# Performance work log

Hardware: AMD Instinct MI355X
Metric: run time of the kernel (lower is better)

## Reference

```python
import jax, jax.numpy as jnp
import numpy as np
import math

N_NODES = 20000
N_EDGES = 320000
NODE_IN = 128
HIDDEN = 64
HEADS = 4
TIME_DIM = 64
SCALE = 60.0 / 1.0  # sensitivity / epsilon


def _linear_params(key, din, dout):
    k1, k2 = jax.random.split(key)
    bound = 1.0 / math.sqrt(din)
    w = jax.random.uniform(k1, (din, dout), minval=-bound, maxval=bound, dtype=jnp.float32)
    b = jax.random.uniform(k2, (dout,), minval=-bound, maxval=bound, dtype=jnp.float32)
    return w, b


def setup_inputs() -> dict:
    key = jax.random.key(0)
    ks = jax.random.split(key, 16)
    edge_index = jax.random.randint(ks[0], (2, N_EDGES), 0, N_NODES, dtype=jnp.int64)
    raw_time = jax.random.uniform(ks[1], (N_EDGES, 1), dtype=jnp.float32) * 86400.0
    noise = jax.random.laplace(ks[2], (N_EDGES, 1), dtype=jnp.float32) * SCALE
    node_emb = jax.random.normal(ks[3], (N_NODES, NODE_IN), dtype=jnp.float32)
    HC = HEADS * HIDDEN
    wq1, bq1 = _linear_params(ks[4], NODE_IN, HC)
    wk1, bk1 = _linear_params(ks[5], NODE_IN, HC)
    wv1, bv1 = _linear_params(ks[6], NODE_IN, HC)
    wt1, bt1 = _linear_params(ks[7], TIME_DIM, HC)
    wq2, bq2 = _linear_params(ks[8], HC, HC)
    wk2, bk2 = _linear_params(ks[9], HC, HC)
    wv2, bv2 = _linear_params(ks[10], HC, HC)
    wt2, bt2 = _linear_params(ks[11], TIME_DIM, HC)
    wc, bc = _linear_params(ks[12], HC, 1)
    return dict(edge_index=edge_index, raw_time=raw_time, noise=noise, node_emb=node_emb,
                wq1=wq1, bq1=bq1, wk1=wk1, bk1=bk1, wv1=wv1, bv1=bv1, wt1=wt1, bt1=bt1,
                wq2=wq2, bq2=bq2, wk2=wk2, bk2=bk2, wv2=wv2, bv2=bv2, wt2=wt2, bt2=bt2,
                wc=wc, bc=bc)


def time_encode(t):
    # t: [E, 1] -> [E, TIME_DIM]; interleaved sin/cos as in TimeEncoder
    half = jnp.arange(0, TIME_DIM, 2, dtype=jnp.float32)
    div_term = jnp.exp(half * (-math.log(10000.0) / TIME_DIM))  # [TIME_DIM/2]
    arg = t * div_term  # [E, TIME_DIM/2]
    te = jnp.stack([jnp.sin(arg), jnp.cos(arg)], axis=-1)  # [E, T/2, 2]
    return te.reshape(t.shape[0], TIME_DIM)


def temporal_conv(x, src, dst, time_enc, wq, bq, wk, bk, wv, bv, wt, bt):
    # gather-QKV, edge softmax over dst segments, scatter-add aggregation
    N = x.shape[0]
    q = (x @ wq + bq).reshape(N, HEADS, HIDDEN)
    k = (x @ wk + bk).reshape(N, HEADS, HIDDEN)
    v = (x @ wv + bv).reshape(N, HEADS, HIDDEN)
    t_enc = (time_enc @ wt + bt).reshape(-1, HEADS, HIDDEN)  # [E,H,C]
    q_i = q[dst]                      # [E,H,C]
    k_j = k[src] + t_enc              # [E,H,C]
    alpha = (q_i * k_j).sum(-1) / math.sqrt(HIDDEN)  # [E,H]
    # segment softmax over index = dst (PyG softmax semantics)
    amax = jax.ops.segment_max(alpha, dst, num_segments=N)  # [N,H]
    ea = jnp.exp(alpha - amax[dst])
    denom = jax.ops.segment_sum(ea, dst, num_segments=N)
    alpha = ea / (denom[dst] + 1e-16)
    msg = v[src] * alpha[..., None]   # [E,H,C]
    out = jax.ops.segment_sum(msg, dst, num_segments=N)  # [N,H,C]
    return out.reshape(N, HEADS * HIDDEN)


def reference(edge_index, raw_time, noise, node_emb,
              wq1, bq1, wk1, bk1, wv1, bv1, wt1, bt1,
              wq2, bq2, wk2, bk2, wv2, bv2, wt2, bt2,
              wc, bc):
    src, dst = edge_index[0], edge_index[1]
    noisy_time = raw_time + noise                 # Laplace mechanism
    time_encoded = time_encode(noisy_time)        # [E, TIME_DIM]
    x = jax.nn.relu(temporal_conv(node_emb, src, dst, time_encoded,
                                  wq1, bq1, wk1, bk1, wv1, bv1, wt1, bt1))
    x = jax.nn.relu(temporal_conv(x, src, dst, time_encoded,
                                  wq2, bq2, wk2, bk2, wv2, bv2, wt2, bt2))
    edge_emb = x[src] + x[dst]                    # [E, H*C]
    out = edge_emb @ wc + bc                      # [E, 1]
    return out.squeeze(-1)
```

## Files before the change

### kernel.cpp

```cpp
#include <hip/hip_runtime.h>
#include <hip/hip_fp16.h>
#include <math.h>

#define NN   20000
#define NE   320000
#define NIN  128
#define HC   256
#define NB   1024

#define AGG_BLOCKS 2500
#define AGG_STRIDE 10000
#define LOG2E_8    0.18033688f

#define GEMM_BLOCKS 1280
#define GEMM_RT     157

typedef unsigned short u16;
typedef __attribute__((ext_vector_type(8))) short bf16x8;
typedef __attribute__((ext_vector_type(4))) float f32x4;

__device__ __forceinline__ float bf2f(u16 u) {
  union { unsigned int i; float f; } x;
  x.i = ((unsigned int)u) << 16;
  return x.f;
}
__device__ __forceinline__ u16 f2bf(float f) {
  union { float f; unsigned int i; } x;
  x.f = f;
  unsigned int r = x.i + 0x7fffu + ((x.i >> 16) & 1u);
  return (u16)(r >> 16);
}
__device__ __forceinline__ float bflo(int v) {
  union { int i; float f; } x; x.i = v << 16; return x.f;
}
__device__ __forceinline__ float bfhi(int v) {
  union { int i; float f; } x; x.i = v & 0xffff0000; return x.f;
}

__device__ __forceinline__ float ldf(const void* p, int i, bool fbf) {
  return fbf ? bf2f(((const u16*)p)[i]) : ((const float*)p)[i];
}
__device__ __forceinline__ int ldsrc(const void* p, int e, bool is64) {
  const int* p32 = (const int*)p;
  return is64 ? p32[2 * e] : p32[e];
}
__device__ __forceinline__ int lddst(const void* p, int e, bool is64) {
  const int* p32 = (const int*)p;
  return is64 ? p32[2 * (NE + e)] : p32[NE + e];
}
__device__ __forceinline__ void stout(void* p, int i, float v, bool fbf) {
  if (fbf) ((u16*)p)[i] = f2bf(v);
  else ((float*)p)[i] = v;
}

__device__ __forceinline__ void gload_lds16(const u16* g, u16* l) {
  __builtin_amdgcn_global_load_lds(
      (const __attribute__((address_space(1))) void*)g,
      (__attribute__((address_space(3))) void*)l, 16, 0, 0);
}

__device__ __forceinline__ float dpp_row_allsum(float s) {
  union fi { float f; int i; };
  fi a, b;
  a.f = s;
  b.i = __builtin_amdgcn_update_dpp(0, a.i, 0x121, 0xf, 0xf, true); a.f += b.f;
  b.i = __builtin_amdgcn_update_dpp(0, a.i, 0x122, 0xf, 0xf, true); a.f += b.f;
  b.i = __builtin_amdgcn_update_dpp(0, a.i, 0x124, 0xf, 0xf, true); a.f += b.f;
  b.i = __builtin_amdgcn_update_dpp(0, a.i, 0x128, 0xf, 0xf, true); a.f += b.f;
  return a.f;
}

__device__ __forceinline__ float fexp2(float x) {
#if __has_builtin(__builtin_amdgcn_exp2f)
  return __builtin_amdgcn_exp2f(x);
#else
  return exp2f(x);
#endif
}

#if __has_builtin(__builtin_amdgcn_fdot2_f32_bf16)
#define HAS_BF16_DOT2 1
typedef __attribute__((ext_vector_type(2))) __bf16 bfv2_t;
__device__ __forceinline__ float qkdot2(int a, int b, float c) {
  return __builtin_amdgcn_fdot2_f32_bf16(__builtin_bit_cast(bfv2_t, a),
                                         __builtin_bit_cast(bfv2_t, b), c, false);
}
#else
#define HAS_BF16_DOT2 0
#endif

__device__ __forceinline__ void edge_do(int2 kk, int2 vv, float tt, int2 q2,
    float dc0, float dc1,
    float qsx, float qsy, float qsz, float qsw,
    float px, float py, float pz, float pw, float qb,
    float& denom, float& a0, float& a1, float& a2, float& a3) {
  const float CH = 0.15915494f;
  const float CL = (float)(0.15915494309189535 - (double)0.15915494f);
  float x0 = tt * dc0, x1 = tt * dc1;
  float p0 = x0 * CH, p1 = x1 * CH;
  float e0 = fmaf(x0, CH, -p0), e1 = fmaf(x1, CH, -p1);
  e0 = fmaf(x0, CL, e0);  e1 = fmaf(x1, CL, e1);
  float fr0 = (p0 - rintf(p0)) + e0;
  float fr1 = (p1 - rintf(p1)) + e1;
  float sv0 = __builtin_amdgcn_sinf(fr0), cv0 = __builtin_amdgcn_cosf(fr0);
  float sv1 = __builtin_amdgcn_sinf(fr1), cv1 = __builtin_amdgcn_cosf(fr1);
  float stp = sv0 * px + cv0 * py + sv1 * pz + cv1 * pw;
#if HAS_BF16_DOT2
  float sqk = qkdot2(kk.y, q2.y, qkdot2(kk.x, q2.x, 0.f));
  float partial = sqk * LOG2E_8 + stp;
#else
  float partial = stp + qsx * bflo(kk.x) + qsy * bfhi(kk.x) +
                  qsz * bflo(kk.y) + qsw * bfhi(kk.y);
#endif
  float a = dpp_row_allsum(partial) + qb;
  float ea = fexp2(a);
  denom += ea;
  a0 = fmaf(ea, bflo(vv.x), a0);
  a1 = fmaf(ea, bfhi(vv.x), a1);
  a2 = fmaf(ea, bflo(vv.y), a2);
  a3 = fmaf(ea, bfhi(vv.y), a3);
}

__global__ void devinit_zero_kernel(const void* __restrict__ eidx,
                                    const void* __restrict__ nemb,
                                    int* __restrict__ flags, float* __restrict__ divt,
                                    int* __restrict__ cursor) {
  int i = blockIdx.x * 256 + threadIdx.x;
  if (i < NN) cursor[i] = 0;
  if (blockIdx.x == 0) {
    int lane = threadIdx.x;
    if (lane < 32) {
      const float c32 = (float)(-0.14391156831212787);
      float prod = (float)(2 * lane) * c32;
      divt[lane] = (float)exp((double)prod);
    }
    if (lane == 0) {
      const int* p32 = (const int*)eidx;
      int is64 = 1;
      for (int k = 1; k < 128; k += 2)
        if (p32[k] != 0) { is64 = 0; break; }
      const u16* q16 = (const u16*)nemb;
      int fbf = 1;
      for (int k = 0; k < 128; k += 2) {
        unsigned e = (q16[k] >> 7) & 0xFF;
        if (e < 90 || e > 140) { fbf = 0; break; }
      }
      flags[0] = is64;
      flags[1] = fbf;
    }
  }
}

__global__ void sentinel_kernel(const int* __restrict__ flags, void* __restrict__ out) {
  int i = blockIdx.x * 256 + threadIdx.x;
  if (i < NE) stout(out, i, 3000.0f, flags[1] != 0);
}
__global__ void raw_sentinel_kernel(u16* __restrict__ out) {
  int i = blockIdx.x * 256 + threadIdx.x;
  if (i < NE) out[i] = f2bf(3000.0f);
}

__global__ void hist_cast_kernel(const int* __restrict__ flags, const void* __restrict__ eidx,
                                 int* __restrict__ cnt, const void* __restrict__ nemb,
                                 u16* __restrict__ acast) {
  bool is64 = flags[0] != 0;
  int b = blockIdx.x, t = threadIdx.x;
  if (b < (NE / 256)) {
    int e = b * 256 + t;
    int d = lddst(eidx, e, is64);
    if ((unsigned)d < NN) atomicAdd(&cnt[d], 1);
  }
  if (!flags[1]) {
    int i = b * 256 + t;
    if (i < NN * NIN / 4) {
      float4 v = ((const float4*)nemb)[i];
      ushort4 o;
      o.x = f2bf(v.x); o.y = f2bf(v.y); o.z = f2bf(v.z); o.w = f2bf(v.w);
      ((ushort4*)acast)[i] = o;
    }
  }
}

__global__ __launch_bounds__(1024) void scanall_kernel(int* __restrict__ cnt_cursor,
                                                       int* __restrict__ offs) {
  __shared__ int s[1024];
  int t = threadIdx.x;
  const int PER = (NN + 1023) / 1024;
  int base = t * PER;
  int loc[PER];
  int sum = 0;
#pragma unroll
  for (int i = 0; i < PER; ++i) {
    int idx = base + i;
    int v = (idx < NN) ? cnt_cursor[idx] : 0;
    loc[i] = sum;
    sum += v;
  }
  s[t] = sum;
  __syncthreads();
  for (int off = 1; off < 1024; off <<= 1) {
    int y = (t >= off) ? s[t - off] : 0;
    __syncthreads();
    s[t] += y;
    __syncthreads();
  }
  int tbase = s[t] - sum;
#pragma unroll
  for (int i = 0; i < PER; ++i) {
    int idx = base + i;
    if (idx < NN) {
      int v = tbase + loc[i];
      offs[idx] = v;
      cnt_cursor[idx] = v;
    }
  }
  if (t == 1023) offs[NN] = s[t];
}

__global__ void fill_kernel(const int* __restrict__ flags, const void* __restrict__ eidx,
                            const void* __restrict__ rawt, const void* __restrict__ noise,
                            int* __restrict__ cursor, int* __restrict__ ssrc,
                            float* __restrict__ stt) {
  bool is64 = flags[0] != 0, fbf = flags[1] != 0;
  int e = blockIdx.x * 256 + threadIdx.x;
  if (e < NE) {
    int d = lddst(eidx, e, is64);
    if ((unsigned)d < NN) {
      int pos = atomicAdd(&cursor[d], 1);
      if ((unsigned)pos < NE) {
        int src = ldsrc(eidx, e, is64);
        if ((unsigned)src >= NN) src = 0;
        ssrc[pos] = src;
        stt[pos] = ldf(rawt, e, fbf) + ldf(noise, e, fbf);
      }
    }
  }
}

__global__ void transw3_kernel(const int* __restrict__ flags, const void* __restrict__ W0,
                               const void* __restrict__ W1, const void* __restrict__ W2,
                               u16* __restrict__ WtBig, int K) {
  bool fbf = flags[1] != 0;
  __shared__ u16 tile[64][65];
  int z = blockIdx.z;
  const void* W = (z == 0) ? W0 : (z == 1) ? W1 : W2;
  u16* dst = WtBig + (size_t)z * 256 * K;
  int kb = blockIdx.x * 64, cb = blockIdx.y * 64;
  int tx = threadIdx.x & 63, ty = threadIdx.x >> 6;
  for (int i = ty; i < 64; i += 4)
    tile[tx][i] = f2bf(ldf(W, (kb + i) * HC + cb + tx, fbf));
  __syncthreads();
  for (int i = ty; i < 64; i += 4)
    dst[(size_t)(cb + i) * K + kb + tx] = tile[i][tx];
}

__global__ void wcombbias_kernel(const int* __restrict__ flags, const void* __restrict__ wt,
                                 const u16* __restrict__ Wqt, u16* __restrict__ Wout,
                                 const void* __restrict__ bq, const void* __restrict__ bk,
                                 const void* __restrict__ bv, float* __restrict__ biasBig,
                                 int K) {
  bool fbf = flags[1] != 0;
  int b = blockIdx.x, t = threadIdx.x;
  if (b < 256) {
    __shared__ float wrow[64];
    int j = b, h = j >> 6;
    if (t < 64) wrow[t] = ldf(wt, (j & 63) * HC + h * 64 + t, fbf);
    __syncthreads();
    if (t < K) {
      float s = 0.f;
#pragma unroll 8
      for (int mm = 0; mm < 64; ++mm)
        s += wrow[mm] * bf2f(Wqt[(size_t)(h * 64 + mm) * K + t]);
      Wout[(size_t)j * K + t] = f2bf(s);
    }
  } else if (b < 259) {
    int bb = b - 256;
    const void* p = (bb == 0) ? bq : (bb == 1) ? bk : bv;
    biasBig[bb * 256 + t] = ldf(p, t, fbf);
  } else {
    int j = t, h = j >> 6;
    float s = 0.f;
    for (int mm = 0; mm < 64; ++mm)
      s += ldf(bq, h * 64 + mm, fbf) * ldf(wt, (j & 63) * HC + h * 64 + mm, fbf);
    biasBig[768 + j] = s;
  }
}

template <int KT, bool AWS>
__global__ __launch_bounds__(256) void gemm_mfma(
    const int* __restrict__ flags, const void* __restrict__ Ap,
    const u16* __restrict__ Acast, const u16* __restrict__ Wt,
    const float* __restrict__ bias, u16* __restrict__ C, int M) {
  bool fbf = flags[1] != 0;
  const u16* A = AWS ? (const u16*)Ap : (fbf ? (const u16*)Ap : Acast);

  int lid = blockIdx.x;
  int xcd = lid & 7;
  int j = lid >> 3;
  int rl = j >> 3, col = j & 7;
  const int qr = GEMM_RT >> 3, rem = GEMM_RT & 7;
  int nrows = qr + (xcd < rem ? 1 : 0);
  if (rl >= nrows) return;
  int row = xcd * qr + (xcd < rem ? xcd : rem) + rl;
  int rb = row * 128, cb = col * 128;

  __shared__ u16 As[128 * 128];
  __shared__ u16 Bs[128 * 128];
  int tid = threadIdx.x;
  int wave = tid >> 6, lane = tid & 63;
  int l15 = lane & 15, quad = lane >> 4;
  int mbase = (wave >> 1) * 64, nbase = (wave & 1) * 64;

  f32x4 acc[4][4];
#pragma unroll
  for (int mt = 0; mt < 4; ++mt)
#pragma unroll
    for (int nt = 0; nt < 4; ++nt)
#pragma unroll
      for (int r = 0; r < 4; ++r) acc[mt][nt][r] = 0.f;

  int srow0 = tid >> 2, schunk0 = tid & 3;
  int srow1 = (tid + 256) >> 2, schunk1 = (tid + 256) & 3;
  int gchunk0 = schunk0 ^ (srow0 & 3);
  int gchunk1 = schunk1 ^ (srow1 & 3);
  int arow0 = rb + srow0; if (arow0 >= M) arow0 = M - 1;
  int arow1 = rb + srow1; if (arow1 >= M) arow1 = M - 1;
  int slo0 = srow0 * 32 + schunk0 * 8;
  int slo1 = srow1 * 32 + schunk1 * 8;
  const u16* bsrc0 = Wt + (size_t)(cb + srow0) * KT + gchunk0 * 8;
  const u16* bsrc1 = Wt + (size_t)(cb + srow1) * KT + gchunk1 * 8;
  const u16* asrc0 = A + (size_t)arow0 * KT + gchunk0 * 8;
  const u16* asrc1 = A + (size_t)arow1 * KT + gchunk1 * 8;

#pragma unroll
  for (int sl = 0; sl < KT / 128; ++sl) {
    if (sl) __syncthreads();
#pragma unroll
    for (int s = 0; s < 4; ++s) {
      int kk = sl * 128 + s * 32;
      int sb = s * 4096;
      gload_lds16(asrc0 + kk, &As[sb + slo0]);
      gload_lds16(asrc1 + kk, &As[sb + slo1]);
      gload_lds16(bsrc0 + kk, &Bs[sb + slo0]);
      gload_lds16(bsrc1 + kk, &Bs[sb + slo1]);
    }
    __syncthreads();
#pragma unroll
    for (int s = 0; s < 4; ++s) {
      int sb = s * 4096;
      bf16x8 bfrag[4];
#pragma unroll
      for (int nt = 0; nt < 4; ++nt) {
        int col2 = nbase + nt * 16 + l15;
        bfrag[nt] = *(const bf16x8*)&Bs[sb + col2 * 32 + ((quad ^ (col2 & 3)) * 8)];
      }
#pragma unroll
      for (int mt = 0; mt < 4; ++mt) {
        int row2 = mbase + mt * 16 + l15;
        bf16x8 afrag = *(const bf16x8*)&As[sb + row2 * 32 + ((quad ^ (row2 & 3)) * 8)];
#pragma unroll
        for (int nt = 0; nt < 4; ++nt)
          acc[mt][nt] = __builtin_amdgcn_mfma_f32_16x16x32_bf16(afrag, bfrag[nt], acc[mt][nt], 0, 0, 0);
      }
    }
  }

  float bvv[4];
#pragma unroll
  for (int nt = 0; nt < 4; ++nt) bvv[nt] = bias[cb + nbase + nt * 16 + l15];
#pragma unroll
  for (int mt = 0; mt < 4; ++mt) {
#pragma unroll
    for (int r = 0; r < 4; ++r) {
      int grow = rb + mbase + mt * 16 + quad * 4 + r;
      if (grow < M) {
        size_t rowo = (size_t)grow * NB + cb + nbase + l15;
#pragma unroll
        for (int nt = 0; nt < 4; ++nt)
          C[rowo + nt * 16] = f2bf(acc[mt][nt][r] + bvv[nt]);
      }
    }
  }
}

template <int DOY>
__global__ __launch_bounds__(256) void aggfused_kernel(
    const int* __restrict__ flags, const int* __restrict__ ssrc,
    const int* __restrict__ offsets, const float* __restrict__ stt,
    const float* __restrict__ divt,
    const u16* __restrict__ qkvp, const void* __restrict__ bt,
    u16* __restrict__ xout, const void* __restrict__ wc,
    float* __restrict__ ynode) {
  bool fbf = flags[1] != 0;
  int lane = threadIdx.x & 63;
  int c = lane * 4;

  int i0 = (2 * lane) & 31;
  float dc0 = divt[i0], dc1 = divt[i0 + 1];
  float btv0 = ldf(bt, c + 0, fbf), btv1 = ldf(bt, c + 1, fbf);
  float btv2 = ldf(bt, c + 2, fbf), btv3 = ldf(bt, c + 3, fbf);
  float wcv0 = 0.f, wcv1 = 0.f, wcv2 = 0.f, wcv3 = 0.f;
  if (DOY) {
    wcv0 = ldf(wc, c + 0, fbf); wcv1 = ldf(wc, c + 1, fbf);
    wcv2 = ldf(wc, c + 2, fbf); wcv3 = ldf(wc, c + 3, fbf);
  }

  int n = blockIdx.x * 4 + (threadIdx.x >> 6);
  int s0 = offsets[n], s1 = offsets[n + 1];
  int2 q2 = *(const int2*)(qkvp + (size_t)n * NB + c);
  int2 p2 = *(const int2*)(qkvp + (size_t)n * NB + 768 + c);

  while (n < NN) {
    int n1 = n + AGG_STRIDE;
    int n1c = (n1 < NN) ? n1 : 0;
    int s0n = offsets[n1c], s1n = offsets[n1c + 1];
    int2 q2n = *(const int2*)(qkvp + (size_t)n1c * NB + c);
    int2 p2n = *(const int2*)(qkvp + (size_t)n1c * NB + 768 + c);

    float qx = bflo(q2.x), qy = bfhi(q2.x), qz = bflo(q2.y), qw = bfhi(q2.y);
    float px = bflo(p2.x) * LOG2E_8, py = bfhi(p2.x) * LOG2E_8;
    float pz = bflo(p2.y) * LOG2E_8, pw = bfhi(p2.y) * LOG2E_8;
    float pb = qx * btv0 + qy * btv1 + qz * btv2 + qw * btv3;
    float qb = dpp_row_allsum(pb) * LOG2E_8;
    float qsx = qx * LOG2E_8, qsy = qy * LOG2E_8;
    float qsz = qz * LOG2E_8, qsw = qw * LOG2E_8;

    float denom = 0.f, acc0 = 0.f, acc1 = 0.f, acc2 = 0.f, acc3 = 0.f;
    const int* sp = ssrc + s0;
    const float* tp = stt + s0;
    int ecnt = s1 - s0;
    int e = 0;
    if (ecnt >= 4) {
      int sA = sp[0], sB = sp[1], sC = sp[2], sD = sp[3];
      while (e + 4 <= ecnt) {
        const u16* bA = qkvp + ((unsigned)sA << 10) + c;
        const u16* bB = qkvp + ((unsigned)sB << 10) + c;
        const u16* bC = qkvp + ((unsigned)sC << 10) + c;
        const u16* bD = qkvp + ((unsigned)sD << 10) + c;
        int2 kA = *(const int2*)(bA + 256), vA = *(const int2*)(bA + 512);
        int2 kB = *(const int2*)(bB + 256), vB = *(const int2*)(bB + 512);
        int2 kC = *(const int2*)(bC + 256), vC = *(const int2*)(bC + 512);
        int2 kD = *(const int2*)(bD + 256), vD = *(const int2*)(bD + 512);
        float ttA = tp[e], ttB = tp[e + 1], ttC = tp[e + 2], ttD = tp[e + 3];
        int en = e + 4;
        if (en + 4 <= ecnt) {
          sA = sp[en]; sB = sp[en + 1]; sC = sp[en + 2]; sD = sp[en + 3];
        }
        edge_do(kA, vA, ttA, q2, dc0, dc1, qsx, qsy, qsz, qsw, px, py, pz, pw, qb,
                denom, acc0, acc1, acc2, acc3);
        edge_do(kB, vB, ttB, q2, dc0, dc1, qsx, qsy, qsz, qsw, px, py, pz, pw, qb,
                denom, acc0, acc1, acc2, acc3);
        edge_do(kC, vC, ttC, q2, dc0, dc1, qsx, qsy, qsz, qsw, px, py, pz, pw, qb,
                denom, acc0, acc1, acc2, acc3);
        edge_do(kD, vD, ttD, q2, dc0, dc1, qsx, qsy, qsz, qsw, px, py, pz, pw, qb,
                denom, acc0, acc1, acc2, acc3);
        e = en;
      }
    }
    for (; e < ecnt; ++e) {
      int s = sp[e];
      const u16* bS = qkvp + ((unsigned)s << 10) + c;
      int2 kS = *(const int2*)(bS + 256), vS = *(const int2*)(bS + 512);
      float tt = tp[e];
      edge_do(kS, vS, tt, q2, dc0, dc1, qsx, qsy, qsz, qsw, px, py, pz, pw, qb,
              denom, acc0, acc1, acc2, acc3);
    }

    float inv = 1.f / (denom + 1e-16f);
    ushort4 r;
    r.x = f2bf(fmaxf(acc0 * inv, 0.f));
    r.y = f2bf(fmaxf(acc1 * inv, 0.f));
    r.z = f2bf(fmaxf(acc2 * inv, 0.f));
    r.w = f2bf(fmaxf(acc3 * inv, 0.f));
    *(ushort4*)(xout + (size_t)n * HC + c) = r;
    if (DOY) {
      float yv = bf2f(r.x) * wcv0 + bf2f(r.y) * wcv1 +
                 bf2f(r.z) * wcv2 + bf2f(r.w) * wcv3;
      yv = dpp_row_allsum(yv);
      yv += __shfl_xor(yv, 16);
      yv += __shfl_xor(yv, 32);
      if (lane == 0) ynode[n] = yv;
    }

    n = n1;
    s0 = s0n; s1 = s1n; q2 = q2n; p2 = p2n;
  }
}

__global__ __launch_bounds__(256) void final2_kernel(
    const int* __restrict__ flags, const void* __restrict__ eidx,
    const float* __restrict__ y, const void* __restrict__ bc,
    void* __restrict__ out) {
  bool is64 = flags[0] != 0, fbf = flags[1] != 0;
  int e = blockIdx.x * 256 + threadIdx.x;
  if (e >= NE) return;
  int src = ldsrc(eidx, e, is64);
  int dst = lddst(eidx, e, is64);
  if ((unsigned)src >= NN) src = 0;
  if ((unsigned)dst >= NN) dst = 0;
  stout(out, e, y[src] + y[dst] + ldf(bc, 0, fbf), fbf);
}

extern "C" void kernel_launch(void* const* d_in, const int* in_sizes, int n_in,
                              void* d_out, int out_size, void* d_ws, size_t ws_size,
                              hipStream_t stream) {
  const void* eidx  = d_in[0];
  const void* rawt  = d_in[1];
  const void* noise = d_in[2];
  const void* nemb  = d_in[3];
  const void *wq1 = d_in[4],  *bq1 = d_in[5];
  const void *wk1 = d_in[6],  *bk1 = d_in[7];
  const void *wv1 = d_in[8],  *bv1 = d_in[9];
  const void *wt1 = d_in[10], *bt1 = d_in[11];
  const void *wq2 = d_in[12], *bq2 = d_in[13];
  const void *wk2 = d_in[14], *bk2 = d_in[15];
  const void *wv2 = d_in[16], *bv2 = d_in[17];
  const void *wt2 = d_in[18], *bt2 = d_in[19];
  const void *wcp = d_in[20], *bcp = d_in[21];

  char* ws = (char*)d_ws;
  size_t off = 0;
  auto alloc = [&](size_t bytes) -> void* {
    void* p = ws + off;
    off += (bytes + 255) & ~(size_t)255;
    return p;
  };
  int*   flags  = (int*)alloc(256);
  float* divt   = (float*)alloc(256);
  u16*   WtBig  = (u16*)alloc((size_t)NB * HC * 2);
  float* biasBig= (float*)alloc((size_t)NB * 4);
  u16*   qkvp   = (u16*)alloc((size_t)NN * NB * 2);
  u16*   x1     = (u16*)alloc((size_t)NN * HC * 2);
  u16*   x2     = (u16*)alloc((size_t)NN * HC * 2);
  u16*   acast  = (u16*)alloc((size_t)NN * NIN * 2);
  float* ynode  = (float*)alloc((size_t)NN * 4);
  int* offsets  = (int*)alloc((size_t)(NN + 1) * 4);
  int* cursor   = (int*)alloc((size_t)NN * 4);
  int* ssrc     = (int*)alloc((size_t)NE * 4);
  float* stt    = (float*)alloc((size_t)NE * 4);
  size_t need = off;

  int gN = (NN + 255) / 256, gE = (NE + 255) / 256;

  if (ws_size < 1024) {
    raw_sentinel_kernel<<<gE, 256, 0, stream>>>((u16*)d_out);
    return;
  }
  devinit_zero_kernel<<<gN, 256, 0, stream>>>(eidx, nemb, flags, divt, cursor);
  if (need > ws_size) {
    sentinel_kernel<<<gE, 256, 0, stream>>>(flags, d_out);
    return;
  }

  hist_cast_kernel<<<(NN * NIN / 4 + 255) / 256, 256, 0, stream>>>(flags, eidx, cursor,
                                                                   nemb, acast);
  scanall_kernel<<<1, 1024, 0, stream>>>(cursor, offsets);
  fill_kernel<<<gE, 256, 0, stream>>>(flags, eidx, rawt, noise, cursor, ssrc, stt);

  dim3 gt1(NIN / 64, 4, 3), gt2(HC / 64, 4, 3);

  transw3_kernel<<<gt1, 256, 0, stream>>>(flags, wq1, wk1, wv1, WtBig, NIN);
  wcombbias_kernel<<<260, 256, 0, stream>>>(flags, wt1, WtBig, WtBig + (size_t)768 * NIN,
                                            bq1, bk1, bv1, biasBig, NIN);
  gemm_mfma<NIN, false><<<GEMM_BLOCKS, 256, 0, stream>>>(flags, nemb, acast, WtBig,
                                                         biasBig, qkvp, NN);
  aggfused_kernel<0><<<AGG_BLOCKS, 256, 0, stream>>>(flags, ssrc, offsets, stt, divt,
                                                     qkvp, bt1, x1, wcp, ynode);

  transw3_kernel<<<gt2, 256, 0, stream>>>(flags, wq2, wk2, wv2, WtBig, HC);
  wcombbias_kernel<<<260, 256, 0, stream>>>(flags, wt2, WtBig, WtBig + (size_t)768 * HC,
                                            bq2, bk2, bv2, biasBig, HC);
  gemm_mfma<HC, true><<<GEMM_BLOCKS, 256, 0, stream>>>(flags, x1, (const u16*)0, WtBig,
                                                       biasBig, qkvp, NN);
  aggfused_kernel<1><<<AGG_BLOCKS, 256, 0, stream>>>(flags, ssrc, offsets, stt, divt,
                                                     qkvp, bt2, x2, wcp, ynode);

  final2_kernel<<<gE, 256, 0, stream>>>(flags, eidx, ynode, bcp, d_out);
}
```

Baseline: 338.7 us.

## Double-buffer GEMM K-slices in LDS to overlap loads with MFMA

Replaces the single 64KB LDS staging of whole 128-wide K slices with a two-buffer ring of 32-wide K chunks, issuing the next chunk's global-to-LDS loads while MFMAs run on the current one. K becomes a runtime argument instead of a template parameter. This cuts LDS use per block, which should allow more resident blocks, and hides load latency. The cost is more barriers, a non-unrolled K loop and less instruction-level parallelism per stage.

```diff
diff --git a/kernel.cpp b/kernel.cpp
--- a/kernel.cpp
+++ b/kernel.cpp
@@ -286,11 +286,11 @@
   }
 }
 
-template <int KT, bool AWS>
+template <bool AWS>
 __global__ __launch_bounds__(256) void gemm_mfma(
     const int* __restrict__ flags, const void* __restrict__ Ap,
     const u16* __restrict__ Acast, const u16* __restrict__ Wt,
-    const float* __restrict__ bias, u16* __restrict__ C, int M) {
+    const float* __restrict__ bias, u16* __restrict__ C, int M, int K) {
   bool fbf = flags[1] != 0;
   const u16* A = AWS ? (const u16*)Ap : (fbf ? (const u16*)Ap : Acast);
 
@@ -304,8 +304,8 @@
   int row = xcd * qr + (xcd < rem ? xcd : rem) + rl;
   int rb = row * 128, cb = col * 128;
 
-  __shared__ u16 As[128 * 128];
-  __shared__ u16 Bs[128 * 128];
+  __shared__ u16 As[2][128 * 32];
+  __shared__ u16 Bs[2][128 * 32];
   int tid = threadIdx.x;
   int wave = tid >> 6, lane = tid & 63;
   int l15 = lane & 15, quad = lane >> 4;
@@ -327,43 +327,45 @@
   int arow1 = rb + srow1; if (arow1 >= M) arow1 = M - 1;
   int slo0 = srow0 * 32 + schunk0 * 8;
   int slo1 = srow1 * 32 + schunk1 * 8;
-  const u16* bsrc0 = Wt + (size_t)(cb + srow0) * KT + gchunk0 * 8;
-  const u16* bsrc1 = Wt + (size_t)(cb + srow1) * KT + gchunk1 * 8;
-  const u16* asrc0 = A + (size_t)arow0 * KT + gchunk0 * 8;
-  const u16* asrc1 = A + (size_t)arow1 * KT + gchunk1 * 8;
-
-#pragma unroll
-  for (int sl = 0; sl < KT / 128; ++sl) {
-    if (sl) __syncthreads();
-#pragma unroll
-    for (int s = 0; s < 4; ++s) {
-      int kk = sl * 128 + s * 32;
-      int sb = s * 4096;
-      gload_lds16(asrc0 + kk, &As[sb + slo0]);
-      gload_lds16(asrc1 + kk, &As[sb + slo1]);
-      gload_lds16(bsrc0 + kk, &Bs[sb + slo0]);
-      gload_lds16(bsrc1 + kk, &Bs[sb + slo1]);
-    }
+  const u16* bsrc0 = Wt + (size_t)(cb + srow0) * K + gchunk0 * 8;
+  const u16* bsrc1 = Wt + (size_t)(cb + srow1) * K + gchunk1 * 8;
+  const u16* asrc0 = A + (size_t)arow0 * K + gchunk0 * 8;
+  const u16* asrc1 = A + (size_t)arow1 * K + gchunk1 * 8;
+
+  auto STAGE = [&](int b, int kk) {
+    gload_lds16(asrc0 + kk, &As[b][slo0]);
+    gload_lds16(asrc1 + kk, &As[b][slo1]);
+    gload_lds16(bsrc0 + kk, &Bs[b][slo0]);
+    gload_lds16(bsrc1 + kk, &Bs[b][slo1]);
+  };
+
+  auto COMPUTE = [&](int b) {
+    bf16x8 bfrag[4];
+#pragma unroll
+    for (int nt = 0; nt < 4; ++nt) {
+      int col2 = nbase + nt * 16 + l15;
+      bfrag[nt] = *(const bf16x8*)&Bs[b][col2 * 32 + ((quad ^ (col2 & 3)) * 8)];
+    }
+#pragma unroll
+    for (int mt = 0; mt < 4; ++mt) {
+      int row2 = mbase + mt * 16 + l15;
+      bf16x8 afrag = *(const bf16x8*)&As[b][row2 * 32 + ((quad ^ (row2 & 3)) * 8)];
+#pragma unroll
+      for (int nt = 0; nt < 4; ++nt)
+        acc[mt][nt] = __builtin_amdgcn_mfma_f32_16x16x32_bf16(afrag, bfrag[nt], acc[mt][nt], 0, 0, 0);
+    }
+  };
+
+  STAGE(0, 0);
+  __syncthreads();
+  int cur = 0;
+  for (int kk = 32; kk < K; kk += 32) {
+    STAGE(cur ^ 1, kk);
+    COMPUTE(cur);
     __syncthreads();
-#pragma unroll
-    for (int s = 0; s < 4; ++s) {
-      int sb = s * 4096;
-      bf16x8 bfrag[4];
-#pragma unroll
-      for (int nt = 0; nt < 4; ++nt) {
-        int col2 = nbase + nt * 16 + l15;
-        bfrag[nt] = *(const bf16x8*)&Bs[sb + col2 * 32 + ((quad ^ (col2 & 3)) * 8)];
-      }
-#pragma unroll
-      for (int mt = 0; mt < 4; ++mt) {
-        int row2 = mbase + mt * 16 + l15;
-        bf16x8 afrag = *(const bf16x8*)&As[sb + row2 * 32 + ((quad ^ (row2 & 3)) * 8)];
-#pragma unroll
-        for (int nt = 0; nt < 4; ++nt)
-          acc[mt][nt] = __builtin_amdgcn_mfma_f32_16x16x32_bf16(afrag, bfrag[nt], acc[mt][nt], 0, 0, 0);
-      }
-    }
-  }
+    cur ^= 1;
+  }
+  COMPUTE(cur);
 
   float bvv[4];
 #pragma unroll
@@ -562,16 +564,16 @@
   transw3_kernel<<<gt1, 256, 0, stream>>>(flags, wq1, wk1, wv1, WtBig, NIN);
   wcombbias_kernel<<<260, 256, 0, stream>>>(flags, wt1, WtBig, WtBig + (size_t)768 * NIN,
                                             bq1, bk1, bv1, biasBig, NIN);
-  gemm_mfma<NIN, false><<<GEMM_BLOCKS, 256, 0, stream>>>(flags, nemb, acast, WtBig,
-                                                         biasBig, qkvp, NN);
+  gemm_mfma<false><<<GEMM_BLOCKS, 256, 0, stream>>>(flags, nemb, acast, WtBig, biasBig,
+                                                    qkvp, NN, NIN);
   aggfused_kernel<0><<<AGG_BLOCKS, 256, 0, stream>>>(flags, ssrc, offsets, stt, divt,
                                                      qkvp, bt1, x1, wcp, ynode);
 
   transw3_kernel<<<gt2, 256, 0, stream>>>(flags, wq2, wk2, wv2, WtBig, HC);
   wcombbias_kernel<<<260, 256, 0, stream>>>(flags, wt2, WtBig, WtBig + (size_t)768 * HC,
                                             bq2, bk2, bv2, biasBig, HC);
-  gemm_mfma<HC, true><<<GEMM_BLOCKS, 256, 0, stream>>>(flags, x1, (const u16*)0, WtBig,
-                                                       biasBig, qkvp, NN);
+  gemm_mfma<true><<<GEMM_BLOCKS, 256, 0, stream>>>(flags, x1, (const u16*)0, WtBig, biasBig,
+                                                   qkvp, NN, HC);
   aggfused_kernel<1><<<AGG_BLOCKS, 256, 0, stream>>>(flags, ssrc, offsets, stt, divt,
                                                      qkvp, bt2, x2, wcp, ynode);
 
```

Result: no change. 341.5 us (+0.8%).
